# Kernel optimization log

Measured on AMD Instinct MI355X. Metric: run time of the kernel, lower is better.

Reference implementation:

```python
import jax, jax.numpy as jnp
import numpy as np

B, S, D = 4, 2048, 1024
LAYERS = 2
NLOPS = 4
GAMMA = 0.01          # lindblad_gamma
COND_TH = 100.0       # condition_threshold
EPS = 1e-6


def setup_inputs() -> dict:
    key = jax.random.key(0)
    ks = jax.random.split(key, 9)
    x_real = jax.random.normal(ks[0], (B, S, D), jnp.float32)
    x_imag = jax.random.normal(ks[1], (B, S, D), jnp.float32)
    H_prev = jax.random.uniform(ks[2], (B, D, D), jnp.float32)
    eye = jnp.eye(D, dtype=jnp.float32)
    # base mixing layer (stand-in for ComplexMamba3Layer): near-identity complex linear
    W_real = eye[None, :, :] + 0.02 * jax.random.normal(ks[3], (LAYERS, D, D), jnp.float32)
    W_imag = 0.02 * jax.random.normal(ks[4], (LAYERS, D, D), jnp.float32)
    L_ops = 0.5 * jax.random.normal(ks[5], (LAYERS, NLOPS, D), jnp.float32)
    theta = jax.random.uniform(ks[6], (LAYERS,), jnp.float32, 0.0, 0.5)
    jump_scale = 0.9 * jnp.ones((LAYERS,), jnp.float32)
    kappa_th = 0.1 * jnp.ones((LAYERS,), jnp.float32)   # curvature_threshold per layer
    return dict(x_real=x_real, x_imag=x_imag, H_prev=H_prev,
                W_real=W_real, W_imag=W_imag, L_ops=L_ops,
                theta=theta, jump_scale=jump_scale, kappa_th=kappa_th)


def _v8_forward(x_real, x_imag, H_prev, W_real, W_imag, L_ops, theta, jump_scale, kappa_th):
    psi = jax.lax.complex(x_real, x_imag)  # [B,S,D] complex64
    Hp = H_prev                            # [B,D,D] real (prev Hamiltonian, detached)
    for l in range(LAYERS):
        residual = psi
        # --- base layer: complex linear mix ---
        Wc = jax.lax.complex(W_real[l], W_imag[l])
        out = jnp.einsum('bsd,de->bse', psi, Wc)
        branch_delta = out - residual
        # --- delta-RMS normalize (no_grad -> stop_gradient) ---
        rms = jnp.sqrt(jnp.clip(jnp.mean(branch_delta.real ** 2 + branch_delta.imag ** 2), 1e-12, None))
        rms = jax.lax.stop_gradient(jnp.maximum(rms, 1e-3))
        b = branch_delta / rms
        # --- Lindblad dissipation: diagonal damping gamma * sum_k L_k^2 ---
        damp = GAMMA * jnp.sum(L_ops[l] ** 2, axis=0)  # [D]
        b = b * (1.0 - damp)
        # --- approximate Hamiltonian H = (1/S) sum_s |psi_s><psi_s| (no_grad) ---
        mag = jnp.abs(b)                                # [B,S,D]
        H = jax.lax.stop_gradient(jnp.einsum('bsd,bse->bde', mag, mag) / S)  # [B,D,D]
        # --- hybrid automata: curvature K = ||H - Hp||_F / ||Hp||_F ---
        diff_n = jnp.sqrt(jnp.sum((H - Hp) ** 2, axis=(1, 2)))
        prev_n = jnp.sqrt(jnp.sum(Hp ** 2, axis=(1, 2)))
        K = diff_n / (prev_n + EPS)                     # [B]
        jumped = K > kappa_th[l]
        b = jnp.where(jumped[:, None, None], b * jump_scale[l].astype(jnp.complex64), b)
        Hp = H
        # --- quaternionic escape: diag-based condition estimate, phase rotation ---
        dg = jnp.diagonal(H, axis1=1, axis2=2)          # [B,D]
        cond = jnp.max(dg, axis=1) / (jnp.min(dg, axis=1) + 1e-12)
        escaped = cond > COND_TH
        rot = jnp.exp(1j * theta[l]).astype(jnp.complex64)
        b = jnp.where(escaped[:, None, None], b * rot, b)
        # --- rescale and residual ---
        b = b * rms
        psi = residual + b
    return jnp.stack([psi.real, psi.imag], axis=0)  # [2,B,S,D] float32


def reference(x_real, x_imag, H_prev, W_real, W_imag, L_ops, theta, jump_scale, kappa_th):
    return _v8_forward(x_real, x_imag, H_prev, W_real, W_imag, L_ops, theta, jump_scale, kappa_th)
```

## Files before the change

kernel.cpp:

```cpp
#include <hip/hip_runtime.h>

#define B_ 4
#define S_ 2048
#define D_ 1024
#define M_ (B_*S_)
#define K2_ 2048
#define N2_ 2048
#define NTOT (B_*S_*D_)
#define DD (D_*D_)

typedef __attribute__((ext_vector_type(4))) float f32x4;
typedef __attribute__((ext_vector_type(8))) short short8;
typedef __attribute__((ext_vector_type(4))) unsigned short u16x4;

static __device__ __forceinline__ unsigned short f2bf(float f) {
    union { float f; unsigned int u; } v; v.f = f;
    unsigned int u = v.u;
    unsigned int r = (u + 0x7fffu + ((u >> 16) & 1u)) >> 16;
    return (unsigned short)r;
}
static __device__ __forceinline__ float bf2f(unsigned short h) {
    union { unsigned int u; float f; } v; v.u = ((unsigned int)h) << 16;
    return v.f;
}


__device__ __forceinline__ void mfma_gemm_128(const unsigned short* __restrict__ Ag, long astride,
                                              const unsigned short* __restrict__ Bg, long bstride,
                                              int kiters,
                                              unsigned short* As, unsigned short* Bs,
                                              f32x4 acc[4][4])
{
    const int tid  = threadIdx.x;
    const int wave = tid >> 6, lane = tid & 63;
    const int q    = lane >> 4, lm = lane & 15;
    const int wm   = (wave >> 1) * 64, wn = (wave & 1) * 64;
    const int crow = lane >> 3;
    const int gcol = ((lane & 7) ^ crow) * 8;

    for (int kt = 0; kt < kiters; ++kt) {
        const long k0 = (long)kt * 64;
        __syncthreads();
#pragma unroll
        for (int i2 = 0; i2 < 4; ++i2) {
            int c   = i2 * 4 + wave;
            int row = c * 8 + crow;
            const unsigned short* ga = Ag + (long)row * astride + k0 + gcol;
            const unsigned short* gb = Bg + (long)row * bstride + k0 + gcol;
            __builtin_amdgcn_global_load_lds((const __attribute__((address_space(1))) void*)ga,
                                             (__attribute__((address_space(3))) void*)(As + c * 512),
                                             16, 0, 0);
            __builtin_amdgcn_global_load_lds((const __attribute__((address_space(1))) void*)gb,
                                             (__attribute__((address_space(3))) void*)(Bs + c * 512),
                                             16, 0, 0);
        }
        __syncthreads();
#pragma unroll
        for (int kk = 0; kk < 64; kk += 32) {
            short8 a[4], b[4];
#pragma unroll
            for (int t = 0; t < 4; ++t) {
                int arow  = wm + t * 16 + lm;
                int aslot = ((kk >> 3) + q) ^ (arow & 7);
                a[t] = *(const short8*)(As + arow * 64 + aslot * 8);
                int brow  = wn + t * 16 + lm;
                int bslot = ((kk >> 3) + q) ^ (brow & 7);
                b[t] = *(const short8*)(Bs + brow * 64 + bslot * 8);
            }
#pragma unroll
            for (int um = 0; um < 4; ++um)
#pragma unroll
                for (int un = 0; un < 4; ++un)
                    acc[um][un] = __builtin_amdgcn_mfma_f32_16x16x32_bf16(a[um], b[un], acc[um][un], 0, 0, 0);
        }
    }
}

__device__ __forceinline__ void mfma_gemm_64(const unsigned short* __restrict__ Ag, long astride,
                                             const unsigned short* __restrict__ Bg, long bstride,
                                             int kiters,
                                             unsigned short* As, unsigned short* Bs,
                                             f32x4 acc[2][2])
{
    const int tid  = threadIdx.x;
    const int wave = tid >> 6, lane = tid & 63;
    const int q    = lane >> 4, lm = lane & 15;
    const int wm   = (wave >> 1) * 32, wn = (wave & 1) * 32;
    const int crow = lane >> 3;
    const int gcol = ((lane & 7) ^ crow) * 8;

    for (int kt = 0; kt < kiters; ++kt) {
        const long k0 = (long)kt * 64;
        __syncthreads();
#pragma unroll
        for (int i2 = 0; i2 < 2; ++i2) {
            int c   = i2 * 4 + wave;
            int row = c * 8 + crow;
            const unsigned short* ga = Ag + (long)row * astride + k0 + gcol;
            const unsigned short* gb = Bg + (long)row * bstride + k0 + gcol;
            __builtin_amdgcn_global_load_lds((const __attribute__((address_space(1))) void*)ga,
                                             (__attribute__((address_space(3))) void*)(As + c * 512),
                                             16, 0, 0);
            __builtin_amdgcn_global_load_lds((const __attribute__((address_space(1))) void*)gb,
                                             (__attribute__((address_space(3))) void*)(Bs + c * 512),
                                             16, 0, 0);
        }
        __syncthreads();
#pragma unroll
        for (int kk = 0; kk < 64; kk += 32) {
            short8 a[2], b[2];
#pragma unroll
            for (int t = 0; t < 2; ++t) {
                int arow  = wm + t * 16 + lm;
                int aslot = ((kk >> 3) + q) ^ (arow & 7);
                a[t] = *(const short8*)(As + arow * 64 + aslot * 8);
                int brow  = wn + t * 16 + lm;
                int bslot = ((kk >> 3) + q) ^ (brow & 7);
                b[t] = *(const short8*)(Bs + brow * 64 + bslot * 8);
            }
#pragma unroll
            for (int um = 0; um < 2; ++um)
#pragma unroll
                for (int un = 0; un < 2; ++un)
                    acc[um][un] = __builtin_amdgcn_mfma_f32_16x16x32_bf16(a[um], b[un], acc[um][un], 0, 0, 0);
        }
    }
}

__global__ __launch_bounds__(256) void gemm_main(const unsigned short* __restrict__ A2,
                                                 const unsigned short* __restrict__ B2T,
                                                 unsigned short* __restrict__ bd2,
                                                 float* __restrict__ scal, int l)
{
    __shared__ unsigned short As[128 * 64];
    __shared__ unsigned short Bs[128 * 64];
    __shared__ float red[4];
    f32x4 acc[4][4];
#pragma unroll
    for (int i = 0; i < 4; ++i)
#pragma unroll
        for (int j = 0; j < 4; ++j) acc[i][j] = (f32x4)0.0f;

    const int nt = blockIdx.x, mt = blockIdx.y;
    mfma_gemm_128(A2 + (long)mt * 128 * K2_, K2_,
                  B2T + (long)nt * 128 * K2_, K2_, K2_ / 64, As, Bs, acc);

    const int tid = threadIdx.x, wave = tid >> 6, lane = tid & 63;
    const int q = lane >> 4, lm = lane & 15;
    const int wm = (wave >> 1) * 64, wn = (wave & 1) * 64;
    float ss = 0.f;
#pragma unroll
    for (int um = 0; um < 4; ++um) {
#pragma unroll
        for (int un = 0; un < 4; ++un) {
            int coln = nt * 128 + wn + un * 16 + lm;
#pragma unroll
            for (int i = 0; i < 4; ++i) {
                int rowm = mt * 128 + wm + um * 16 + q * 4 + i;
                float bd = acc[um][un][i];
                bd2[(long)rowm * N2_ + coln] = f2bf(bd);
                ss += bd * bd;
            }
        }
    }
    for (int off = 32; off > 0; off >>= 1) ss += __shfl_down(ss, off);
    if (lane == 0) red[wave] = ss;
    __syncthreads();
    if (tid == 0) atomicAdd(scal + l, red[0] + red[1] + red[2] + red[3]);
}

__global__ __launch_bounds__(256) void gemm_H(const unsigned short* __restrict__ magT,
                                              const float* __restrict__ Hp,
                                              float* __restrict__ H,
                                              float* __restrict__ scal, int l)
{
    __shared__ unsigned short As[64 * 64];
    __shared__ unsigned short Bs[64 * 64];
    __shared__ float redd[4], redp[4];
    f32x4 acc[2][2];
#pragma unroll
    for (int i = 0; i < 2; ++i)
#pragma unroll
        for (int j = 0; j < 2; ++j) acc[i][j] = (f32x4)0.0f;

    const int b = blockIdx.z;
    const unsigned short* Mb = magT + (long)b * D_ * S_;
    mfma_gemm_64(Mb + (long)blockIdx.y * 64 * S_, S_,
                 Mb + (long)blockIdx.x * 64 * S_, S_, S_ / 64, As, Bs, acc);

    const int tid = threadIdx.x, wave = tid >> 6, lane = tid & 63;
    const int q = lane >> 4, lm = lane & 15;
    const int wm = (wave >> 1) * 32, wn = (wave & 1) * 32;
    const float inv_s = 1.0f / (float)S_;
    float d2 = 0.f, p2 = 0.f;
#pragma unroll
    for (int um = 0; um < 2; ++um) {
#pragma unroll
        for (int un = 0; un < 2; ++un) {
            int coln = blockIdx.x * 64 + wn + un * 16 + lm;
#pragma unroll
            for (int i = 0; i < 4; ++i) {
                int rowm = blockIdx.y * 64 + wm + um * 16 + q * 4 + i;
                long adr = (long)b * DD + (long)rowm * D_ + coln;
                float hp = Hp[adr];
                float h  = acc[um][un][i] * inv_s;
                H[adr] = h;
                float df = h - hp;
                d2 += df * df;
                p2 += hp * hp;
                if (rowm == coln) {
                    atomicMax((int*)scal + 18 + l * 4 + b, __float_as_int(h));
                    atomicMin((int*)scal + 26 + l * 4 + b, __float_as_int(h));
                }
            }
        }
    }
    for (int off = 32; off > 0; off >>= 1) { d2 += __shfl_down(d2, off); p2 += __shfl_down(p2, off); }
    if (lane == 0) { redd[wave] = d2; redp[wave] = p2; }
    __syncthreads();
    if (tid == 0) {
        atomicAdd(scal + 2 + l * 4 + b,  redd[0] + redd[1] + redd[2] + redd[3]);
        atomicAdd(scal + 10 + l * 4 + b, redp[0] + redp[1] + redp[2] + redp[3]);
    }
}

__global__ void init_kernel(const float* __restrict__ xr, const float* __restrict__ xi,
                            float* __restrict__ psi_r, float* __restrict__ psi_i,
                            unsigned short* __restrict__ A2, float* __restrict__ scal)
{
    if (blockIdx.x == 0 && threadIdx.x < 34)
        scal[threadIdx.x] = (threadIdx.x >= 26) ? 3.402823466e38f : 0.0f;
    long t = (long)blockIdx.x * 256 + threadIdx.x;
    long i = t * 4;
    f32x4 r  = *(const f32x4*)(xr + i);
    f32x4 im = *(const f32x4*)(xi + i);
    *(f32x4*)(psi_r + i) = r;
    *(f32x4*)(psi_i + i) = im;
    long m = i / D_; int d = (int)(i % D_);
    u16x4 rr, ii;
#pragma unroll
    for (int j = 0; j < 4; ++j) { rr[j] = f2bf(r[j]); ii[j] = f2bf(im[j]); }
    *(u16x4*)(A2 + m * K2_ + d) = rr;
    *(u16x4*)(A2 + m * K2_ + D_ + d) = ii;
}

__global__ __launch_bounds__(256) void pack_b2t(const float* __restrict__ Wr_all,
                                                const float* __restrict__ Wi_all,
                                                unsigned short* __restrict__ B2T_all)
{
    __shared__ float T[64][65];
    const int l = blockIdx.z;
    const float* Wr = Wr_all + (long)l * DD;
    const float* Wi = Wi_all + (long)l * DD;
    unsigned short* B2T = B2T_all + (long)l * N2_ * K2_;
    int k0 = blockIdx.x * 64;
    int n0 = blockIdx.y * 64;
    int t = threadIdx.x;
#pragma unroll
    for (int it = 0; it < 16; ++it) {
        int idx = it * 256 + t;
        int kl = idx >> 6, nl = idx & 63;
        int k = k0 + kl, n = n0 + nl;
        float v;
        if (k < D_) v = (n < D_) ? Wr[k * D_ + n] : Wi[k * D_ + (n - D_)];
        else        v = (n < D_) ? -Wi[(k - D_) * D_ + n] : Wr[(k - D_) * D_ + (n - D_)];
        if (k == n) v -= 1.0f;
        T[kl][nl] = v;
    }
    __syncthreads();
#pragma unroll
    for (int it = 0; it < 16; ++it) {
        int idx = it * 256 + t;
        int nl = idx >> 6, kl = idx & 63;
        B2T[(long)(n0 + nl) * K2_ + (k0 + kl)] = f2bf(T[kl][nl]);
    }
}

__global__ void damp_kernel(const float* __restrict__ Lops, float* __restrict__ dampv)
{
    int g = blockIdx.x;
    int l = g >> 2;
    int d = (g & 3) * 256 + threadIdx.x;
    const float* Lp = Lops + (long)l * 4 * D_;
    float s = 0.f;
#pragma unroll
    for (int k = 0; k < 4; ++k) { float v = Lp[k * D_ + d]; s += v * v; }
    dampv[l * D_ + d] = 1.0f - 0.01f * s;
}

__global__ __launch_bounds__(256) void magt_kernel(const unsigned short* __restrict__ bd2,
                                                   const float* __restrict__ dampv,
                                                   const float* __restrict__ scal, int l,
                                                   unsigned short* __restrict__ magT)
{
    __shared__ float T[64][65];
    float mean = fmaxf(scal[l] / (float)NTOT, 1e-12f);
    const float inv = 1.0f / fmaxf(sqrtf(mean), 1e-3f);
    int m0 = blockIdx.x * 64;
    int d0 = blockIdx.y * 64;
    int t = threadIdx.x;
#pragma unroll
    for (int it = 0; it < 16; ++it) {
        int idx = it * 256 + t;
        int sl = idx >> 6, dl = idx & 63;
        long m = m0 + sl; int d = d0 + dl;
        float br = bf2f(bd2[m * N2_ + d]);
        float bi = bf2f(bd2[m * N2_ + D_ + d]);
        T[sl][dl] = sqrtf(br * br + bi * bi) * dampv[d] * inv;
    }
    __syncthreads();
    int b = m0 / S_;
    int s0 = m0 % S_;
#pragma unroll
    for (int it = 0; it < 16; ++it) {
        int idx = it * 256 + t;
        int dl = idx >> 6, sl = idx & 63;
        magT[(long)b * D_ * S_ + (long)(d0 + dl) * S_ + (s0 + sl)] = f2bf(T[sl][dl]);
    }
}

__global__ void update_kernel(const unsigned short* __restrict__ bd2,
                              const float* __restrict__ dampv,
                              const float* __restrict__ scal,
                              const float* __restrict__ theta,
                              const float* __restrict__ jscale,
                              const float* __restrict__ kappa, int l,
                              float* __restrict__ psi_r,
                              float* __restrict__ psi_i,
                              unsigned short* __restrict__ A2,
                              int write_a2)
{
    long t = (long)blockIdx.x * 256 + threadIdx.x;
    long i = t * 4;
    long m = i / D_; int d = (int)(i % D_);
    int b = (int)(m >> 11);

    float dn = sqrtf(scal[2 + l * 4 + b]);
    float pn = sqrtf(scal[10 + l * 4 + b]);
    float K  = dn / (pn + 1e-6f);
    float mx = __int_as_float(((const int*)scal)[18 + l * 4 + b]);
    float mn = __int_as_float(((const int*)scal)[26 + l * 4 + b]);
    int jumped  = K > kappa[l];
    int escaped = (mx / (mn + 1e-12f)) > 100.0f;
    float js = jumped ? jscale[l] : 1.0f;
    float th = theta[l];
    float fr = js * (escaped ? cosf(th) : 1.0f);
    float fi = js * (escaped ? sinf(th) : 0.0f);

    u16x4 brv = *(const u16x4*)(bd2 + m * N2_ + d);
    u16x4 biv = *(const u16x4*)(bd2 + m * N2_ + D_ + d);
    f32x4 w  = *(const f32x4*)(dampv + d);
    f32x4 pr = *(const f32x4*)(psi_r + i);
    f32x4 pi = *(const f32x4*)(psi_i + i);
    u16x4 ar, ai;
#pragma unroll
    for (int j = 0; j < 4; ++j) {
        float br = bf2f(brv[j]) * w[j];
        float bi = bf2f(biv[j]) * w[j];
        float nr = pr[j] + br * fr - bi * fi;
        float ni = pi[j] + br * fi + bi * fr;
        pr[j] = nr; pi[j] = ni;
        ar[j] = f2bf(nr); ai[j] = f2bf(ni);
    }
    *(f32x4*)(psi_r + i) = pr;
    *(f32x4*)(psi_i + i) = pi;
    if (write_a2) {
        *(u16x4*)(A2 + m * K2_ + d) = ar;
        *(u16x4*)(A2 + m * K2_ + D_ + d) = ai;
    }
}

extern "C" void kernel_launch(void* const* d_in, const int* in_sizes, int n_in,
                              void* d_out, int out_size, void* d_ws, size_t ws_size,
                              hipStream_t stream)
{
    const float* xr     = (const float*)d_in[0];
    const float* xi     = (const float*)d_in[1];
    const float* Hprev  = (const float*)d_in[2];
    const float* Wr     = (const float*)d_in[3];
    const float* Wi     = (const float*)d_in[4];
    const float* Lops   = (const float*)d_in[5];
    const float* theta  = (const float*)d_in[6];
    const float* jscale = (const float*)d_in[7];
    const float* kappa  = (const float*)d_in[8];

    float* psi_r = (float*)d_out;
    float* psi_i = psi_r + NTOT;

    char* ws = (char*)d_ws;
    unsigned short* A2   = (unsigned short*)ws;
    unsigned short* magT = A2;
    unsigned short* B2T  = (unsigned short*)(ws + 33554432);
    unsigned short* bd2  = (unsigned short*)(ws + 50331648);
    float* H             = (float*)(ws + 83886080);
    float* scal          = (float*)(ws + 100663296);
    float* dampv         = scal + 64;

    init_kernel<<<NTOT / 4 / 256, 256, 0, stream>>>(xr, xi, psi_r, psi_i, A2, scal);
    damp_kernel<<<8, 256, 0, stream>>>(Lops, dampv);
    pack_b2t<<<dim3(32, 32, 2), 256, 0, stream>>>(Wr, Wi, B2T);

    for (int l = 0; l < 2; ++l) {
        const float* Hp = (l == 0) ? Hprev : H;
        gemm_main<<<dim3(N2_ / 128, M_ / 128), 256, 0, stream>>>(
            A2, B2T + (long)l * N2_ * K2_, bd2, scal, l);
        magt_kernel<<<dim3(M_ / 64, D_ / 64), 256, 0, stream>>>(
            bd2, dampv + l * D_, scal, l, magT);
        gemm_H<<<dim3(D_ / 64, D_ / 64, B_), 256, 0, stream>>>(magT, Hp, H, scal, l);
        update_kernel<<<NTOT / 4 / 256, 256, 0, stream>>>(
            bd2, dampv + l * D_, scal, theta, jscale, kappa, l,
            psi_r, psi_i, A2, l == 0);
    }
}
```

Before: 510.3 us.

## Fuse magnitude transpose into main GEMM and exploit symmetry of H GEMM

The main complex GEMM now computes real and imaginary output columns in the same block, so it can form |b| in the epilogue and write the transposed bf16 magnitude directly, which removes the separate magt kernel and its re-read of bd2. The rms and damping scaling is moved into the H GEMM epilogue. gemm_H computes only upper-triangular tiles, using the symmetry of H, and mirrors each result to the transposed position. This halves that GEMM's work at the cost of scattered transposed stores. The kernel doubles its accumulators and uses 48KB of LDS, which raises register pressure. B2T packing now runs per layer into a single buffer.

```diff
diff --git a/kernel.cpp b/kernel.cpp
--- a/kernel.cpp
+++ b/kernel.cpp
@@ -12,6 +12,7 @@
 typedef __attribute__((ext_vector_type(4))) float f32x4;
 typedef __attribute__((ext_vector_type(8))) short short8;
 typedef __attribute__((ext_vector_type(4))) unsigned short u16x4;
+typedef __attribute__((ext_vector_type(8))) unsigned short u16x8;
 
 static __device__ __forceinline__ unsigned short f2bf(float f) {
     union { float f; unsigned int u; } v; v.f = f;
@@ -25,39 +26,54 @@
 }
 
 
-__device__ __forceinline__ void mfma_gemm_128(const unsigned short* __restrict__ Ag, long astride,
-                                              const unsigned short* __restrict__ Bg, long bstride,
-                                              int kiters,
-                                              unsigned short* As, unsigned short* Bs,
-                                              f32x4 acc[4][4])
-{
-    const int tid  = threadIdx.x;
-    const int wave = tid >> 6, lane = tid & 63;
-    const int q    = lane >> 4, lm = lane & 15;
-    const int wm   = (wave >> 1) * 64, wn = (wave & 1) * 64;
+__global__ __launch_bounds__(256, 2) void gemm_main2(const unsigned short* __restrict__ A2,
+                                                     const unsigned short* __restrict__ B2T,
+                                                     unsigned short* __restrict__ bd2,
+                                                     unsigned short* __restrict__ magT,
+                                                     float* __restrict__ scal, int l)
+{
+    __shared__ unsigned short smem[3 * 128 * 64];
+    __shared__ float red[4];
+    unsigned short* As  = smem;
+    unsigned short* Bsr = smem + 8192;
+    unsigned short* Bsi = smem + 16384;
+
+    f32x4 accr[4][4], acci[4][4];
+#pragma unroll
+    for (int i = 0; i < 4; ++i)
+#pragma unroll
+        for (int j = 0; j < 4; ++j) { accr[i][j] = (f32x4)0.0f; acci[i][j] = (f32x4)0.0f; }
+
+    const int nt = blockIdx.x, mt = blockIdx.y;
+    const int tid = threadIdx.x, wave = tid >> 6, lane = tid & 63;
+    const int q = lane >> 4, lm = lane & 15;
+    const int wm = (wave >> 1) * 64, wn = (wave & 1) * 64;
     const int crow = lane >> 3;
     const int gcol = ((lane & 7) ^ crow) * 8;
 
-    for (int kt = 0; kt < kiters; ++kt) {
+    const unsigned short* Ag  = A2  + (long)mt * 128 * K2_;
+    const unsigned short* Bgr = B2T + (long)(nt * 128) * K2_;
+    const unsigned short* Bgi = B2T + (long)(nt * 128 + 1024) * K2_;
+
+    for (int kt = 0; kt < K2_ / 64; ++kt) {
         const long k0 = (long)kt * 64;
         __syncthreads();
 #pragma unroll
         for (int i2 = 0; i2 < 4; ++i2) {
             int c   = i2 * 4 + wave;
             int row = c * 8 + crow;
-            const unsigned short* ga = Ag + (long)row * astride + k0 + gcol;
-            const unsigned short* gb = Bg + (long)row * bstride + k0 + gcol;
-            __builtin_amdgcn_global_load_lds((const __attribute__((address_space(1))) void*)ga,
-                                             (__attribute__((address_space(3))) void*)(As + c * 512),
-                                             16, 0, 0);
-            __builtin_amdgcn_global_load_lds((const __attribute__((address_space(1))) void*)gb,
-                                             (__attribute__((address_space(3))) void*)(Bs + c * 512),
-                                             16, 0, 0);
+            long go = (long)row * K2_ + k0 + gcol;
+            __builtin_amdgcn_global_load_lds((const __attribute__((address_space(1))) void*)(Ag + go),
+                                             (__attribute__((address_space(3))) void*)(As + c * 512), 16, 0, 0);
+            __builtin_amdgcn_global_load_lds((const __attribute__((address_space(1))) void*)(Bgr + go),
+                                             (__attribute__((address_space(3))) void*)(Bsr + c * 512), 16, 0, 0);
+            __builtin_amdgcn_global_load_lds((const __attribute__((address_space(1))) void*)(Bgi + go),
+                                             (__attribute__((address_space(3))) void*)(Bsi + c * 512), 16, 0, 0);
         }
         __syncthreads();
 #pragma unroll
         for (int kk = 0; kk < 64; kk += 32) {
-            short8 a[4], b[4];
+            short8 a[4], br[4], bi[4];
 #pragma unroll
             for (int t = 0; t < 4; ++t) {
                 int arow  = wm + t * 16 + lm;
@@ -65,14 +81,56 @@
                 a[t] = *(const short8*)(As + arow * 64 + aslot * 8);
                 int brow  = wn + t * 16 + lm;
                 int bslot = ((kk >> 3) + q) ^ (brow & 7);
-                b[t] = *(const short8*)(Bs + brow * 64 + bslot * 8);
+                br[t] = *(const short8*)(Bsr + brow * 64 + bslot * 8);
+                bi[t] = *(const short8*)(Bsi + brow * 64 + bslot * 8);
             }
 #pragma unroll
             for (int um = 0; um < 4; ++um)
 #pragma unroll
-                for (int un = 0; un < 4; ++un)
-                    acc[um][un] = __builtin_amdgcn_mfma_f32_16x16x32_bf16(a[um], b[un], acc[um][un], 0, 0, 0);
-        }
+                for (int un = 0; un < 4; ++un) {
+                    accr[um][un] = __builtin_amdgcn_mfma_f32_16x16x32_bf16(a[um], br[un], accr[um][un], 0, 0, 0);
+                    acci[um][un] = __builtin_amdgcn_mfma_f32_16x16x32_bf16(a[um], bi[un], acci[um][un], 0, 0, 0);
+                }
+        }
+    }
+
+    __syncthreads();
+    unsigned short* magLds = smem;
+    float ss = 0.f;
+#pragma unroll
+    for (int um = 0; um < 4; ++um) {
+#pragma unroll
+        for (int un = 0; un < 4; ++un) {
+            int colb = wn + un * 16 + lm;
+            int coln = nt * 128 + colb;
+            u16x4 magv;
+#pragma unroll
+            for (int i = 0; i < 4; ++i) {
+                long rowm = (long)mt * 128 + wm + um * 16 + q * 4 + i;
+                float vr = accr[um][un][i];
+                float vi = acci[um][un][i];
+                bd2[rowm * N2_ + coln]        = f2bf(vr);
+                bd2[rowm * N2_ + 1024 + coln] = f2bf(vi);
+                float s2 = vr * vr + vi * vi;
+                ss += s2;
+                magv[i] = f2bf(sqrtf(s2));
+            }
+            *(u16x4*)(magLds + colb * 136 + wm + um * 16 + q * 4) = magv;
+        }
+    }
+    for (int off = 32; off > 0; off >>= 1) ss += __shfl_down(ss, off);
+    if (lane == 0) red[wave] = ss;
+    __syncthreads();
+    if (tid == 0) atomicAdd(scal + l, red[0] + red[1] + red[2] + red[3]);
+
+    const int b   = mt >> 4;
+    const long s0 = (long)(mt & 15) * 128;
+#pragma unroll
+    for (int it = 0; it < 8; ++it) {
+        int sid = it * 256 + tid;
+        int row = sid >> 4, seg = sid & 15;
+        unsigned short* dst = magT + (long)b * D_ * S_ + (long)(nt * 128 + row) * S_ + s0 + seg * 8;
+        *(u16x8*)dst = *(const u16x8*)(magLds + row * 136 + seg * 8);
     }
 }
 
@@ -99,11 +157,9 @@
             const unsigned short* ga = Ag + (long)row * astride + k0 + gcol;
             const unsigned short* gb = Bg + (long)row * bstride + k0 + gcol;
             __builtin_amdgcn_global_load_lds((const __attribute__((address_space(1))) void*)ga,
-                                             (__attribute__((address_space(3))) void*)(As + c * 512),
-                                             16, 0, 0);
+                                             (__attribute__((address_space(3))) void*)(As + c * 512), 16, 0, 0);
             __builtin_amdgcn_global_load_lds((const __attribute__((address_space(1))) void*)gb,
-                                             (__attribute__((address_space(3))) void*)(Bs + c * 512),
-                                             16, 0, 0);
+                                             (__attribute__((address_space(3))) void*)(Bs + c * 512), 16, 0, 0);
         }
         __syncthreads();
 #pragma unroll
@@ -127,90 +183,69 @@
     }
 }
 
-__global__ __launch_bounds__(256) void gemm_main(const unsigned short* __restrict__ A2,
-                                                 const unsigned short* __restrict__ B2T,
-                                                 unsigned short* __restrict__ bd2,
-                                                 float* __restrict__ scal, int l)
-{
-    __shared__ unsigned short As[128 * 64];
-    __shared__ unsigned short Bs[128 * 64];
-    __shared__ float red[4];
-    f32x4 acc[4][4];
-#pragma unroll
-    for (int i = 0; i < 4; ++i)
-#pragma unroll
-        for (int j = 0; j < 4; ++j) acc[i][j] = (f32x4)0.0f;
-
-    const int nt = blockIdx.x, mt = blockIdx.y;
-    mfma_gemm_128(A2 + (long)mt * 128 * K2_, K2_,
-                  B2T + (long)nt * 128 * K2_, K2_, K2_ / 64, As, Bs, acc);
-
-    const int tid = threadIdx.x, wave = tid >> 6, lane = tid & 63;
-    const int q = lane >> 4, lm = lane & 15;
-    const int wm = (wave >> 1) * 64, wn = (wave & 1) * 64;
-    float ss = 0.f;
-#pragma unroll
-    for (int um = 0; um < 4; ++um) {
-#pragma unroll
-        for (int un = 0; un < 4; ++un) {
-            int coln = nt * 128 + wn + un * 16 + lm;
-#pragma unroll
-            for (int i = 0; i < 4; ++i) {
-                int rowm = mt * 128 + wm + um * 16 + q * 4 + i;
-                float bd = acc[um][un][i];
-                bd2[(long)rowm * N2_ + coln] = f2bf(bd);
-                ss += bd * bd;
-            }
-        }
-    }
-    for (int off = 32; off > 0; off >>= 1) ss += __shfl_down(ss, off);
-    if (lane == 0) red[wave] = ss;
-    __syncthreads();
-    if (tid == 0) atomicAdd(scal + l, red[0] + red[1] + red[2] + red[3]);
-}
-
 __global__ __launch_bounds__(256) void gemm_H(const unsigned short* __restrict__ magT,
                                               const float* __restrict__ Hp,
                                               float* __restrict__ H,
-                                              float* __restrict__ scal, int l)
+                                              float* __restrict__ scal,
+                                              const float* __restrict__ dampv, int l)
 {
     __shared__ unsigned short As[64 * 64];
     __shared__ unsigned short Bs[64 * 64];
     __shared__ float redd[4], redp[4];
+
+    int idx = blockIdx.x, ty = 0;
+    while (idx >= 16 - ty) { idx -= 16 - ty; ++ty; }
+    const int tx = ty + idx;
+    const int b = blockIdx.y;
+    const int diag = (tx == ty);
+
     f32x4 acc[2][2];
 #pragma unroll
     for (int i = 0; i < 2; ++i)
 #pragma unroll
         for (int j = 0; j < 2; ++j) acc[i][j] = (f32x4)0.0f;
 
-    const int b = blockIdx.z;
     const unsigned short* Mb = magT + (long)b * D_ * S_;
-    mfma_gemm_64(Mb + (long)blockIdx.y * 64 * S_, S_,
-                 Mb + (long)blockIdx.x * 64 * S_, S_, S_ / 64, As, Bs, acc);
+    mfma_gemm_64(Mb + (long)ty * 64 * S_, S_,
+                 Mb + (long)tx * 64 * S_, S_, S_ / 64, As, Bs, acc);
+
+    float mean = fmaxf(scal[l] / (float)NTOT, 1e-12f);
+    float inv  = 1.0f / fmaxf(sqrtf(mean), 1e-3f);
+    const float scale = inv * inv / (float)S_;
 
     const int tid = threadIdx.x, wave = tid >> 6, lane = tid & 63;
     const int q = lane >> 4, lm = lane & 15;
     const int wm = (wave >> 1) * 32, wn = (wave & 1) * 32;
-    const float inv_s = 1.0f / (float)S_;
     float d2 = 0.f, p2 = 0.f;
 #pragma unroll
     for (int um = 0; um < 2; ++um) {
 #pragma unroll
         for (int un = 0; un < 2; ++un) {
-            int coln = blockIdx.x * 64 + wn + un * 16 + lm;
+            int coln = tx * 64 + wn + un * 16 + lm;
+            float de = dampv[coln];
 #pragma unroll
             for (int i = 0; i < 4; ++i) {
-                int rowm = blockIdx.y * 64 + wm + um * 16 + q * 4 + i;
+                int rowm = ty * 64 + wm + um * 16 + q * 4 + i;
+                float h = acc[um][un][i] * scale * dampv[rowm] * de;
                 long adr = (long)b * DD + (long)rowm * D_ + coln;
-                float hp = Hp[adr];
-                float h  = acc[um][un][i] * inv_s;
-                H[adr] = h;
-                float df = h - hp;
-                d2 += df * df;
-                p2 += hp * hp;
-                if (rowm == coln) {
-                    atomicMax((int*)scal + 18 + l * 4 + b, __float_as_int(h));
-                    atomicMin((int*)scal + 26 + l * 4 + b, __float_as_int(h));
+                float hp1 = Hp[adr];
+                float df1 = h - hp1;
+                if (diag) {
+                    H[adr] = h;
+                    d2 += df1 * df1;
+                    p2 += hp1 * hp1;
+                    if (rowm == coln) {
+                        atomicMax((int*)scal + 18 + l * 4 + b, __float_as_int(h));
+                        atomicMin((int*)scal + 26 + l * 4 + b, __float_as_int(h));
+                    }
+                } else {
+                    long adrT = (long)b * DD + (long)coln * D_ + rowm;
+                    float hp2 = Hp[adrT];
+                    H[adr]  = h;
+                    H[adrT] = h;
+                    float df2 = h - hp2;
+                    d2 += df1 * df1 + df2 * df2;
+                    p2 += hp1 * hp1 + hp2 * hp2;
                 }
             }
         }
@@ -246,13 +281,11 @@
 
 __global__ __launch_bounds__(256) void pack_b2t(const float* __restrict__ Wr_all,
                                                 const float* __restrict__ Wi_all,
-                                                unsigned short* __restrict__ B2T_all)
+                                                unsigned short* __restrict__ B2T, int l)
 {
     __shared__ float T[64][65];
-    const int l = blockIdx.z;
     const float* Wr = Wr_all + (long)l * DD;
     const float* Wi = Wi_all + (long)l * DD;
-    unsigned short* B2T = B2T_all + (long)l * N2_ * K2_;
     int k0 = blockIdx.x * 64;
     int n0 = blockIdx.y * 64;
     int t = threadIdx.x;
@@ -286,37 +319,6 @@
 #pragma unroll
     for (int k = 0; k < 4; ++k) { float v = Lp[k * D_ + d]; s += v * v; }
     dampv[l * D_ + d] = 1.0f - 0.01f * s;
-}
-
-__global__ __launch_bounds__(256) void magt_kernel(const unsigned short* __restrict__ bd2,
-                                                   const float* __restrict__ dampv,
-                                                   const float* __restrict__ scal, int l,
-                                                   unsigned short* __restrict__ magT)
-{
-    __shared__ float T[64][65];
-    float mean = fmaxf(scal[l] / (float)NTOT, 1e-12f);
-    const float inv = 1.0f / fmaxf(sqrtf(mean), 1e-3f);
-    int m0 = blockIdx.x * 64;
-    int d0 = blockIdx.y * 64;
-    int t = threadIdx.x;
-#pragma unroll
-    for (int it = 0; it < 16; ++it) {
-        int idx = it * 256 + t;
-        int sl = idx >> 6, dl = idx & 63;
-        long m = m0 + sl; int d = d0 + dl;
-        float br = bf2f(bd2[m * N2_ + d]);
-        float bi = bf2f(bd2[m * N2_ + D_ + d]);
-        T[sl][dl] = sqrtf(br * br + bi * bi) * dampv[d] * inv;
-    }
-    __syncthreads();
-    int b = m0 / S_;
-    int s0 = m0 % S_;
-#pragma unroll
-    for (int it = 0; it < 16; ++it) {
-        int idx = it * 256 + t;
-        int dl = idx >> 6, sl = idx & 63;
-        magT[(long)b * D_ * S_ + (long)(d0 + dl) * S_ + (s0 + sl)] = f2bf(T[sl][dl]);
-    }
 }
 
 __global__ void update_kernel(const unsigned short* __restrict__ bd2,
@@ -389,24 +391,21 @@
 
     char* ws = (char*)d_ws;
     unsigned short* A2   = (unsigned short*)ws;
-    unsigned short* magT = A2;
     unsigned short* B2T  = (unsigned short*)(ws + 33554432);
-    unsigned short* bd2  = (unsigned short*)(ws + 50331648);
-    float* H             = (float*)(ws + 83886080);
-    float* scal          = (float*)(ws + 100663296);
+    unsigned short* bd2  = (unsigned short*)(ws + 41943040);
+    unsigned short* magT = (unsigned short*)(ws + 75497472);
+    float* H             = (float*)(ws + 92274688);
+    float* scal          = (float*)(ws + 109051904);
     float* dampv         = scal + 64;
 
     init_kernel<<<NTOT / 4 / 256, 256, 0, stream>>>(xr, xi, psi_r, psi_i, A2, scal);
     damp_kernel<<<8, 256, 0, stream>>>(Lops, dampv);
-    pack_b2t<<<dim3(32, 32, 2), 256, 0, stream>>>(Wr, Wi, B2T);
 
     for (int l = 0; l < 2; ++l) {
         const float* Hp = (l == 0) ? Hprev : H;
-        gemm_main<<<dim3(N2_ / 128, M_ / 128), 256, 0, stream>>>(
-            A2, B2T + (long)l * N2_ * K2_, bd2, scal, l);
-        magt_kernel<<<dim3(M_ / 64, D_ / 64), 256, 0, stream>>>(
-            bd2, dampv + l * D_, scal, l, magT);
-        gemm_H<<<dim3(D_ / 64, D_ / 64, B_), 256, 0, stream>>>(magT, Hp, H, scal, l);
+        pack_b2t<<<dim3(32, 32), 256, 0, stream>>>(Wr, Wi, B2T, l);
+        gemm_main2<<<dim3(8, M_ / 128), 256, 0, stream>>>(A2, B2T, bd2, magT, scal, l);
+        gemm_H<<<dim3(136, B_), 256, 0, stream>>>(magT, Hp, H, scal, dampv + l * D_, l);
         update_kernel<<<NTOT / 4 / 256, 256, 0, stream>>>(
             bd2, dampv + l * D_, scal, theta, jscale, kappa, l,
             psi_r, psi_i, A2, l == 0);
```

Measured after the change: 457.5 us. 1.12x faster.
